# Optimization experiments

Measured on AMD Instinct MI355X. Metric: run time of the kernel, lower is better.

## Reference

```python
import jax, jax.numpy as jnp
import numpy as np
from jax import lax

# dims
B, N, D, H, K, NS = 16, 4096, 64, 128, 32, 1024  # clouds, pts/cloud, feat, hidden, max neighbors, fps samples
R = 0.2  # radius


def _fps(pos, n_s):
    """Farthest point sampling on one cloud. pos: [N,3] -> idx [n_s] int32."""
    n = pos.shape[0]

    def step(carry, _):
        dist, last = carry
        d = jnp.sum((pos - pos[last]) ** 2, axis=-1)
        dist = jnp.minimum(dist, d)
        nxt = jnp.argmax(dist).astype(jnp.int32)
        return (dist, nxt), last

    init = (jnp.full((n,), 1e10, pos.dtype), jnp.int32(0))
    _, idx = lax.scan(step, init, None, length=n_s)
    return idx


def setup_inputs() -> dict:
    key = jax.random.key(0)
    ks = jax.random.split(key, 6)
    s1 = 1.0 / np.sqrt(D + 1)
    s2 = 1.0 / np.sqrt(H)
    s3 = 1.0 / np.sqrt(D + H)
    return {
        "x": jax.random.normal(ks[0], (B, N, D), jnp.float32),
        "pos": jax.random.uniform(ks[1], (B, N, 3), jnp.float32),
        "W1": jax.random.normal(ks[2], (D + 1, H), jnp.float32) * s1,
        "b1": jnp.zeros((H,), jnp.float32),
        "W2": jax.random.normal(ks[3], (H, 3), jnp.float32) * s2,
        "b2": jnp.zeros((3,), jnp.float32),
        "W3": jax.random.normal(ks[4], (D + H, H), jnp.float32) * s3,
        "b3": jnp.zeros((H,), jnp.float32),
    }


def reference(x, pos, W1, b1, W2, b2, W3, b3):
    # 1) FPS downsample per cloud -> centers
    idx = jax.vmap(lambda p: _fps(p, NS))(pos)                    # [B,NS]
    pos_s = jax.vmap(lambda p, i: p[i])(pos, idx)                 # [B,NS,3]

    # 2) radius neighbor search: nearest-K within R (<= max_num_neighbors=32)
    d2 = jnp.sum((pos_s[:, :, None, :] - pos[:, None, :, :]) ** 2, axis=-1)  # [B,NS,N]
    masked = jnp.where(d2 <= R * R, d2, jnp.inf)
    neg, nbr = lax.top_k(-masked, K)                              # nearest K
    valid = (-neg) <= R * R                                       # [B,NS,K]

    # 3) gather neighbor features/positions
    x_j = jax.vmap(lambda a, i: a[i])(x, nbr)                     # [B,NS,K,D]
    pos_j = jax.vmap(lambda a, i: a[i])(pos, nbr)                 # [B,NS,K,3]
    diff = pos_j - pos_s[:, :, None, :]                           # pos_j - pos_i
    d2sel = jnp.sum(diff ** 2, axis=-1)
    dist = jnp.where(d2sel > 0, jnp.sqrt(jnp.where(d2sel > 0, d2sel, 1.0)), 0.0)

    # 4) message MLPs
    feat = jnp.concatenate([x_j, dist[..., None]], axis=-1)       # [B,NS,K,D+1]
    emb = jax.nn.relu(feat @ W1 + b1)                             # nn_msg_x
    pw = emb @ W2 + b2                                            # nn_msg_pos
    pmsg = diff * pw

    # 5) masked aggregate: sum for x, mean for pos
    m = valid[..., None].astype(emb.dtype)
    aggr_x = jnp.sum(emb * m, axis=2)                             # [B,NS,H]
    cnt = jnp.maximum(jnp.sum(m, axis=2), 1.0)                    # [B,NS,1]
    aggr_pos = jnp.sum(pmsg * m, axis=2) / cnt                    # [B,NS,3]

    # 6) update
    x_d = jax.vmap(lambda a, i: a[i])(x, idx)                     # [B,NS,D]
    out_x = jax.nn.relu(jnp.concatenate([x_d, aggr_x], axis=-1) @ W3 + b3)
    out_pos = pos_s + aggr_pos
    return out_x, out_pos, idx
```

## Files before the change

### kernel.cpp

```cpp
#include <hip/hip_runtime.h>
#include <math.h>

#define B_ 16
#define N_ 4096
#define D_ 64
#define H_ 128
#define K_ 32
#define NS_ 1024
#define R2_ 0.04f
#define NCAP_ 256
#define NBR_GRID_ ((B_ * NS_) / 4)

typedef short short8 __attribute__((ext_vector_type(8)));
typedef float f32x4 __attribute__((ext_vector_type(4)));
typedef unsigned short ushort_t;

static __device__ __forceinline__ short f2bf(float f) {
    unsigned u = __float_as_uint(f);
    unsigned r = (u + 0x7FFFu + ((u >> 16) & 1u)) >> 16;
    return (short)r;
}

template<int CTRL, int RM>
static __device__ __forceinline__ unsigned dppmov(unsigned v) {
    return (unsigned)__builtin_amdgcn_update_dpp((int)v, (int)v, CTRL, RM, 0xF, false);
}

#define DPP_FMAX_STEP(CTRL, RM)                                           \
    {                                                                     \
        float n = __uint_as_float(dppmov<CTRL, RM>(__float_as_uint(wm))); \
        wm = fmaxf(wm, n);                                                \
    }

#define DPP_UMIN_STEP(CTRL, RM)                                           \
    {                                                                     \
        unsigned n = dppmov<CTRL, RM>(cand);                              \
        cand = n < cand ? n : cand;                                       \
    }

#define DPP_UMIN_STEP_V(var, CTRL, RM)                                    \
    {                                                                     \
        unsigned n = dppmov<CTRL, RM>(var);                               \
        var = n < var ? n : var;                                          \
    }

__global__ __launch_bounds__(256, 1) void fps_kernel(
    const float* __restrict__ pos, int* __restrict__ idx_i,
    float* __restrict__ idx_f, float* __restrict__ pos_s)
{
    __shared__ float4 lpos4[N_];
    __shared__ float4 sres[NS_];
    __shared__ unsigned long long skey[2][4];
    __shared__ float4 scoord[2][4];
    const int b = blockIdx.x;
    const int t = threadIdx.x;
    const int wv = t >> 6;
    const int lane = t & 63;
    const float* posb = pos + (size_t)b * N_ * 3;
    for (int p = t; p < N_; p += 256)
        lpos4[p] = make_float4(posb[3 * p + 0], posb[3 * p + 1], posb[3 * p + 2], 0.f);
    __syncthreads();

    float px[16], py[16], pz[16], dist[16];
#pragma unroll
    for (int j = 0; j < 16; ++j) {
        float4 v = lpos4[t + 256 * j];
        px[j] = v.x; py[j] = v.y; pz[j] = v.z;
        dist[j] = 1e10f;
    }
    unsigned curidx = 0;
    float4 c0 = lpos4[0];
    float ccx = c0.x, ccy = c0.y, ccz = c0.z;

    for (int ns = 0; ns < NS_; ++ns) {
        if (t == 0)
            sres[ns] = make_float4(ccx, ccy, ccz, __uint_as_float(curidx));
        float bv = -1.f; int bj = 0;
#pragma unroll
        for (int j = 0; j < 16; ++j) {
            float dx = __fsub_rn(px[j], ccx);
            float dy = __fsub_rn(py[j], ccy);
            float dz = __fsub_rn(pz[j], ccz);
            float d2 = __fadd_rn(__fadd_rn(__fmul_rn(dx, dx), __fmul_rn(dy, dy)), __fmul_rn(dz, dz));
            float dn = fminf(dist[j], d2);
            dist[j] = dn;
            bool g = dn > bv;
            bv = g ? dn : bv;
            bj = g ? j : bj;
        }
        float wm = bv;
        DPP_FMAX_STEP(0x111, 0xF)
        DPP_FMAX_STEP(0x112, 0xF)
        DPP_FMAX_STEP(0x114, 0xF)
        DPP_FMAX_STEP(0x118, 0xF)
        DPP_FMAX_STEP(0x142, 0xA)
        DPP_FMAX_STEP(0x143, 0xC)
        const float wavemax = __uint_as_float(
            (unsigned)__builtin_amdgcn_readlane((int)__float_as_uint(wm), 63));
        const unsigned pidx = (unsigned)t + ((unsigned)bj << 8);
        const unsigned long long mask = __ballot(bv == wavemax);
        unsigned widx;
        if (__popcll(mask) == 1) {
            const int wl = __ffsll((long long)mask) - 1;
            widx = (unsigned)__builtin_amdgcn_readlane((int)pidx, wl);
        } else {
            unsigned cand = (bv == wavemax) ? pidx : 0xFFFFFFFFu;
            DPP_UMIN_STEP(0x111, 0xF)
            DPP_UMIN_STEP(0x112, 0xF)
            DPP_UMIN_STEP(0x114, 0xF)
            DPP_UMIN_STEP(0x118, 0xF)
            DPP_UMIN_STEP(0x142, 0xA)
            DPP_UMIN_STEP(0x143, 0xC)
            widx = (unsigned)__builtin_amdgcn_readlane((int)cand, 63);
        }
        float4 wc = lpos4[widx];
        if (lane == 0) {
            skey[ns & 1][wv] = (((unsigned long long)__float_as_uint(wavemax)) << 32)
                             | (unsigned long long)(0xFFFFFFFFu - widx);
            scoord[ns & 1][wv] = wc;
        }
        __syncthreads();
        {
            unsigned sid = (unsigned)(lane & 3);
            unsigned long long skv = skey[ns & 1][sid];
            float4 scv = scoord[ns & 1][sid];
            unsigned kh2 = (unsigned)(skv >> 32), kl2 = (unsigned)skv;
#define SLOT_STEP(CTRL)                                                        \
            {                                                                  \
                unsigned nh = dppmov<CTRL, 0xF>(kh2);                          \
                unsigned nl = dppmov<CTRL, 0xF>(kl2);                          \
                unsigned nsid = dppmov<CTRL, 0xF>(sid);                        \
                unsigned long long nk = (((unsigned long long)nh) << 32) | nl; \
                unsigned long long ok = (((unsigned long long)kh2) << 32) | kl2;\
                if (nk > ok) { kh2 = nh; kl2 = nl; sid = nsid; }               \
            }
            SLOT_STEP(0x101)
            SLOT_STEP(0x102)
#undef SLOT_STEP
            const int slotwin = __builtin_amdgcn_readfirstlane((int)sid);
            curidx = 0xFFFFFFFFu - (unsigned)__builtin_amdgcn_readfirstlane((int)kl2);
            ccx = __uint_as_float((unsigned)__builtin_amdgcn_readlane(
                      (int)__float_as_uint(scv.x), slotwin));
            ccy = __uint_as_float((unsigned)__builtin_amdgcn_readlane(
                      (int)__float_as_uint(scv.y), slotwin));
            ccz = __uint_as_float((unsigned)__builtin_amdgcn_readlane(
                      (int)__float_as_uint(scv.z), slotwin));
        }
    }
    __syncthreads();
    for (int i = t; i < NS_; i += 256) {
        float4 r = sres[i];
        unsigned id = __float_as_uint(r.w);
        idx_i[b * NS_ + i] = (int)id;
        idx_f[b * NS_ + i] = (float)id;
        pos_s[(b * NS_ + i) * 3 + 0] = r.x;
        pos_s[(b * NS_ + i) * 3 + 1] = r.y;
        pos_s[(b * NS_ + i) * 3 + 2] = r.z;
    }
}

__global__ __launch_bounds__(256) void nbr_kernel(
    const float* __restrict__ pos, const float* __restrict__ pos_s,
    int* __restrict__ nbr, float* __restrict__ cntv,
    const float* __restrict__ x, ushort_t* __restrict__ xb)
{
    __shared__ unsigned long long ck[4][NCAP_];
    if (blockIdx.x >= NBR_GRID_) {
        const size_t i = ((size_t)(blockIdx.x - NBR_GRID_) * 256 + threadIdx.x) * 8;
        float4 a = *(const float4*)(x + i);
        float4 c = *(const float4*)(x + i + 4);
        short8 o;
        o[0] = f2bf(a.x); o[1] = f2bf(a.y); o[2] = f2bf(a.z); o[3] = f2bf(a.w);
        o[4] = f2bf(c.x); o[5] = f2bf(c.y); o[6] = f2bf(c.z); o[7] = f2bf(c.w);
        *(short8*)(xb + i) = o;
        return;
    }
    const int w = threadIdx.x >> 6;
    const int lane = threadIdx.x & 63;
    const int s = blockIdx.x * 4 + w;
    const int b = s >> 10;
    const float cx = pos_s[s * 3 + 0], cy = pos_s[s * 3 + 1], cz = pos_s[s * 3 + 2];
    const float* posb = pos + (size_t)b * N_ * 3;
    int m = 0;
    for (int base = 0; base < N_; base += 64) {
        int p = base + lane;
        float dx = __fsub_rn(posb[3 * p + 0], cx);
        float dy = __fsub_rn(posb[3 * p + 1], cy);
        float dz = __fsub_rn(posb[3 * p + 2], cz);
        float d2 = __fadd_rn(__fadd_rn(__fmul_rn(dx, dx), __fmul_rn(dy, dy)), __fmul_rn(dz, dz));
        bool in = (d2 <= R2_);
        unsigned long long msk = __ballot(in);
        int before = __popcll(msk & ((1ull << lane) - 1ull));
        int slot = m + before;
        if (in && slot < NCAP_)
            ck[w][slot] = ((unsigned long long)__float_as_uint(d2) << 32) | (unsigned)p;
        m += __popcll(msk);
    }
    __asm__ volatile("s_waitcnt lgkmcnt(0)" ::: "memory");
    int kcnt = m < K_ ? m : K_;
    if (m <= NCAP_) {
        unsigned long long kr[4];
#pragma unroll
        for (int r = 0; r < 4; ++r) {
            int q = r * 64 + lane;
            unsigned long long v = ck[w][q & (NCAP_ - 1)];
            kr[r] = (q < m) ? v : ~0ull;
        }
        unsigned chosen = 0;
        for (int k = 0; k < kcnt; ++k) {
            unsigned long long localk = ~0ull; int br = -1;
#pragma unroll
            for (int r = 0; r < 4; ++r) {
                bool ok = (!((chosen >> r) & 1u)) && (kr[r] < localk);
                localk = ok ? kr[r] : localk;
                br = ok ? r : br;
            }
            const unsigned mybits = (unsigned)(localk >> 32);
            const unsigned myidx = (unsigned)localk;
            unsigned wb = mybits;
            DPP_UMIN_STEP_V(wb, 0x111, 0xF)
            DPP_UMIN_STEP_V(wb, 0x112, 0xF)
            DPP_UMIN_STEP_V(wb, 0x114, 0xF)
            DPP_UMIN_STEP_V(wb, 0x118, 0xF)
            DPP_UMIN_STEP_V(wb, 0x142, 0xA)
            DPP_UMIN_STEP_V(wb, 0x143, 0xC)
            const unsigned minbits = (unsigned)__builtin_amdgcn_readlane((int)wb, 63);
            const unsigned long long wmask = __ballot(mybits == minbits);
            unsigned widx;
            if (__popcll(wmask) == 1) {
                const int wl = __ffsll((long long)wmask) - 1;
                widx = (unsigned)__builtin_amdgcn_readlane((int)myidx, wl);
            } else {
                unsigned cand = (mybits == minbits) ? myidx : 0xFFFFFFFFu;
                DPP_UMIN_STEP(0x111, 0xF)
                DPP_UMIN_STEP(0x112, 0xF)
                DPP_UMIN_STEP(0x114, 0xF)
                DPP_UMIN_STEP(0x118, 0xF)
                DPP_UMIN_STEP(0x142, 0xA)
                DPP_UMIN_STEP(0x143, 0xC)
                widx = (unsigned)__builtin_amdgcn_readlane((int)cand, 63);
            }
            if (mybits == minbits && myidx == widx) chosen |= 1u << br;
            if (lane == 0) nbr[s * K_ + k] = (int)widx;
        }
    } else {
        unsigned long long prev = 0ull;
        for (int k = 0; k < kcnt; ++k) {
            unsigned long long localk = ~0ull;
            for (int base = 0; base < N_; base += 64) {
                int p = base + lane;
                float dx = __fsub_rn(posb[3 * p + 0], cx);
                float dy = __fsub_rn(posb[3 * p + 1], cy);
                float dz = __fsub_rn(posb[3 * p + 2], cz);
                float d2 = __fadd_rn(__fadd_rn(__fmul_rn(dx, dx), __fmul_rn(dy, dy)), __fmul_rn(dz, dz));
                if (d2 <= R2_) {
                    unsigned long long key =
                        ((unsigned long long)__float_as_uint(d2) << 32) | (unsigned)p;
                    if (key >= prev && key < localk) localk = key;
                }
            }
            unsigned kh = (unsigned)(localk >> 32), kl = (unsigned)localk;
#define DPP_MIN_STEP2(CTRL, RM)                                           \
            {                                                             \
                unsigned nh = dppmov<CTRL, RM>(kh);                       \
                unsigned nl = dppmov<CTRL, RM>(kl);                       \
                unsigned long long nk = (((unsigned long long)nh) << 32) | nl; \
                unsigned long long ok = (((unsigned long long)kh) << 32) | kl; \
                if (nk < ok) { kh = nh; kl = nl; }                        \
            }
            DPP_MIN_STEP2(0x111, 0xF)
            DPP_MIN_STEP2(0x112, 0xF)
            DPP_MIN_STEP2(0x114, 0xF)
            DPP_MIN_STEP2(0x118, 0xF)
            DPP_MIN_STEP2(0x142, 0xA)
            DPP_MIN_STEP2(0x143, 0xC)
#undef DPP_MIN_STEP2
            unsigned mh = (unsigned)__builtin_amdgcn_readlane((int)kh, 63);
            unsigned ml = (unsigned)__builtin_amdgcn_readlane((int)kl, 63);
            unsigned long long bk = (((unsigned long long)mh) << 32) | ml;
            prev = bk + 1ull;
            if (lane == 0) nbr[s * K_ + k] = (int)(bk & 0xFFFFFFFFull);
        }
    }
    if (lane == 0) {
        for (int k = kcnt; k < K_; ++k) nbr[s * K_ + k] = -1;
        cntv[s] = (float)kcnt;
    }
}

__global__ __launch_bounds__(256) void msg_kernel(
    const ushort_t* __restrict__ xb, const float* __restrict__ pos,
    const float* __restrict__ W1, const float* __restrict__ b1,
    const float* __restrict__ W2, const float* __restrict__ b2,
    const float* __restrict__ pos_s, const int* __restrict__ nbr,
    const float* __restrict__ cntv, float* __restrict__ aggr_x,
    float* __restrict__ out_pos)
{
    __shared__ __align__(16) char smem[4 * 5120];
    const int t = threadIdx.x;
    const int wv = t >> 6, lane = t & 63;
    const int quad = lane >> 4, cl = lane & 15;
    char* wb = smem + wv * 5120;

    short8 bfrag[8][2];
    float b1v[8], w1dv[8], w2v0[8], w2v1[8], w2v2[8];
#pragma unroll
    for (int Nt = 0; Nt < 8; ++Nt) {
        const int h = Nt * 16 + cl;
#pragma unroll
        for (int ks = 0; ks < 2; ++ks) {
            short8 f;
#pragma unroll
            for (int jj = 0; jj < 8; ++jj)
                f[jj] = f2bf(W1[(ks * 32 + quad * 8 + jj) * H_ + h]);
            bfrag[Nt][ks] = f;
        }
        b1v[Nt] = b1[h];
        w1dv[Nt] = W1[64 * H_ + h];
        w2v0[Nt] = W2[h * 3 + 0];
        w2v1[Nt] = W2[h * 3 + 1];
        w2v2[Nt] = W2[h * 3 + 2];
    }
    const float b20 = b2[0], b21 = b2[1], b22 = b2[2];

    const int kkg = lane >> 1, half = lane & 1;
    for (int i = 0; i < 4; ++i) {
        const int s = blockIdx.x * 16 + wv * 4 + i;
        const int b = s >> 10;
        const int n = nbr[s * K_ + kkg];
        {
            char* frow = wb + kkg * 144 + half * 64;
            if (n >= 0) {
                const short8* xr = (const short8*)(xb + ((size_t)b * N_ + n) * D_) + half * 4;
#pragma unroll
                for (int q = 0; q < 4; ++q) *(short8*)(frow + q * 16) = xr[q];
            } else {
                short8 z = {0, 0, 0, 0, 0, 0, 0, 0};
#pragma unroll
                for (int q = 0; q < 4; ++q) *(short8*)(frow + q * 16) = z;
            }
            if (half == 0) {
                float dxm = 0.f, dym = 0.f, dzm = 0.f, de = -1.f;
                if (n >= 0) {
                    const float* pj = pos + ((size_t)b * N_ + n) * 3;
                    float dx = pj[0] - pos_s[s * 3 + 0];
                    float dy = pj[1] - pos_s[s * 3 + 1];
                    float dz = pj[2] - pos_s[s * 3 + 2];
                    float d2 = dx * dx + dy * dy + dz * dz;
                    de = d2 > 0.f ? sqrtf(d2) : 0.f;
                    dxm = dx; dym = dy; dzm = dz;
                }
                f32x4 sv = {dxm, dym, dzm, de};
                *(f32x4*)(wb + 4608 + kkg * 16) = sv;
            }
        }
        float agp[8] = {0, 0, 0, 0, 0, 0, 0, 0};
        float gp0[8] = {0, 0, 0, 0, 0, 0, 0, 0};
        float gp1[8] = {0, 0, 0, 0, 0, 0, 0, 0};
        float gp2[8] = {0, 0, 0, 0, 0, 0, 0, 0};
#pragma unroll
        for (int Mt = 0; Mt < 2; ++Mt) {
            short8 a0 = *(short8*)(wb + (Mt * 16 + cl) * 144 + quad * 16);
            short8 a1 = *(short8*)(wb + (Mt * 16 + cl) * 144 + 64 + quad * 16);
            f32x4 acc[8];
#pragma unroll
            for (int Nt = 0; Nt < 8; ++Nt) {
                f32x4 z = {0.f, 0.f, 0.f, 0.f};
                z = __builtin_amdgcn_mfma_f32_16x16x32_bf16(a0, bfrag[Nt][0], z, 0, 0, 0);
                z = __builtin_amdgcn_mfma_f32_16x16x32_bf16(a1, bfrag[Nt][1], z, 0, 0, 0);
                acc[Nt] = z;
            }
            f32x4 sd[4];
#pragma unroll
            for (int r = 0; r < 4; ++r)
                sd[r] = *(f32x4*)(wb + 4608 + (Mt * 16 + quad * 4 + r) * 16);
#pragma unroll
            for (int Nt = 0; Nt < 8; ++Nt) {
#pragma unroll
                for (int r = 0; r < 4; ++r) {
                    float dr = sd[r][3];
                    float wgt = dr >= 0.f ? 1.f : 0.f;
                    float dd = dr >= 0.f ? dr : 0.f;
                    float e = fmaf(dd, w1dv[Nt], acc[Nt][r]) + b1v[Nt];
                    e = e > 0.f ? e : 0.f;
                    agp[Nt] = fmaf(wgt, e, agp[Nt]);
                    gp0[Nt] = fmaf(sd[r][0], e, gp0[Nt]);
                    gp1[Nt] = fmaf(sd[r][1], e, gp1[Nt]);
                    gp2[Nt] = fmaf(sd[r][2], e, gp2[Nt]);
                }
            }
        }
#pragma unroll
        for (int Nt = 0; Nt < 8; ++Nt) {
            float v = agp[Nt]; v += __shfl_xor(v, 16); v += __shfl_xor(v, 32);
            aggr_x[(size_t)s * H_ + Nt * 16 + cl] = v;
            float g0 = gp0[Nt]; g0 += __shfl_xor(g0, 16); g0 += __shfl_xor(g0, 32); gp0[Nt] = g0;
            float g1 = gp1[Nt]; g1 += __shfl_xor(g1, 16); g1 += __shfl_xor(g1, 32); gp1[Nt] = g1;
            float g2 = gp2[Nt]; g2 += __shfl_xor(g2, 16); g2 += __shfl_xor(g2, 32); gp2[Nt] = g2;
        }
        float pr0 = 0.f, pr1 = 0.f, pr2 = 0.f;
#pragma unroll
        for (int Nt = 0; Nt < 8; ++Nt) {
            pr0 = fmaf(w2v0[Nt], gp0[Nt], pr0);
            pr1 = fmaf(w2v1[Nt], gp1[Nt], pr1);
            pr2 = fmaf(w2v2[Nt], gp2[Nt], pr2);
        }
#pragma unroll
        for (int off = 1; off < 16; off <<= 1) {
            pr0 += __shfl_xor(pr0, off);
            pr1 += __shfl_xor(pr1, off);
            pr2 += __shfl_xor(pr2, off);
        }
        f32x4 dsv = *(f32x4*)(wb + 4608 + (lane & 31) * 16);
        float q0 = dsv[0], q1 = dsv[1], q2 = dsv[2];
#pragma unroll
        for (int off = 1; off < 32; off <<= 1) {
            q0 += __shfl_xor(q0, off);
            q1 += __shfl_xor(q1, off);
            q2 += __shfl_xor(q2, off);
        }
        float cnt = cntv[s]; if (cnt < 1.f) cnt = 1.f;
        if (lane < 3) {
            float pr = lane == 0 ? pr0 : (lane == 1 ? pr1 : pr2);
            float qq = lane == 0 ? q0 : (lane == 1 ? q1 : q2);
            float bb = lane == 0 ? b20 : (lane == 1 ? b21 : b22);
            out_pos[s * 3 + lane] = pos_s[s * 3 + lane] + (pr + bb * qq) / cnt;
        }
    }
}

__global__ __launch_bounds__(128) void out_kernel(
    const float* __restrict__ x, const float* __restrict__ W3,
    const float* __restrict__ b3, const int* __restrict__ idx_i,
    const float* __restrict__ aggr_x, float* __restrict__ out_x)
{
    __shared__ float rows[32][208];
    const int t = threadIdx.x;
    const int s0 = blockIdx.x * 32;
    const int sl = t >> 2, part = t & 3;
    const int s = s0 + sl;
    const int b = s >> 10;
    const int id = idx_i[s];
    {
        const float4* xr = (const float4*)(x + ((size_t)b * N_ + id) * D_);
        float4* rr = (float4*)&rows[sl][0];
#pragma unroll
        for (int q = 0; q < 4; ++q) rr[part * 4 + q] = xr[part * 4 + q];
        const float4* ar = (const float4*)(aggr_x + (size_t)s * H_);
        float4* rr2 = (float4*)&rows[sl][64];
#pragma unroll
        for (int q = 0; q < 8; ++q) rr2[part * 8 + q] = ar[part * 8 + q];
    }
    __syncthreads();
    float acc[32];
#pragma unroll
    for (int i = 0; i < 32; ++i) acc[i] = 0.f;
    for (int j4 = 0; j4 < 48; ++j4) {
        float w0 = W3[(j4 * 4 + 0) * H_ + t];
        float w1 = W3[(j4 * 4 + 1) * H_ + t];
        float w2 = W3[(j4 * 4 + 2) * H_ + t];
        float w3 = W3[(j4 * 4 + 3) * H_ + t];
#pragma unroll
        for (int i = 0; i < 32; ++i) {
            const float4 f = *(const float4*)&rows[i][j4 * 4];
            float a = acc[i];
            a = fmaf(f.x, w0, a); a = fmaf(f.y, w1, a);
            a = fmaf(f.z, w2, a); a = fmaf(f.w, w3, a);
            acc[i] = a;
        }
    }
    const float bb = b3[t];
#pragma unroll
    for (int i = 0; i < 32; ++i) {
        float v = acc[i] + bb;
        v = v > 0.f ? v : 0.f;
        out_x[(size_t)(s0 + i) * H_ + t] = v;
    }
}

extern "C" void kernel_launch(void* const* d_in, const int* in_sizes, int n_in,
                              void* d_out, int out_size, void* d_ws, size_t ws_size,
                              hipStream_t stream) {
    const float* x   = (const float*)d_in[0];
    const float* pos = (const float*)d_in[1];
    const float* W1  = (const float*)d_in[2];
    const float* b1  = (const float*)d_in[3];
    const float* W2  = (const float*)d_in[4];
    const float* b2  = (const float*)d_in[5];
    const float* W3  = (const float*)d_in[6];
    const float* b3  = (const float*)d_in[7];

    float* out_x   = (float*)d_out;
    float* out_pos = (float*)d_out + 2097152;
    float* idx_f   = (float*)d_out + 2146304;

    char* ws = (char*)d_ws;
    int*      idx_i  = (int*)ws;
    float*    pos_s  = (float*)(ws + 65536);
    int*      nbr    = (int*)(ws + 262144);
    float*    cntv   = (float*)(ws + 2359296);
    float*    aggr_x = (float*)(ws + 2424832);
    ushort_t* x_bf16 = (ushort_t*)(ws + 10813440);

    fps_kernel<<<B_, 256, 0, stream>>>(pos, idx_i, idx_f, pos_s);
    nbr_kernel<<<NBR_GRID_ + (B_ * N_ * D_) / (256 * 8), 256, 0, stream>>>(
        pos, pos_s, nbr, cntv, x, x_bf16);
    msg_kernel<<<(B_ * NS_) / 16, 256, 0, stream>>>(x_bf16, pos, W1, b1, W2, b2,
                                                    pos_s, nbr, cntv, aggr_x, out_pos);
    out_kernel<<<(B_ * NS_) / 32, 128, 0, stream>>>(x, W3, b3, idx_i, aggr_x, out_x);
}
```

Before: 920.3 us.

## Fuse FPS with neighbor search via producer-consumer progress counters

Merges the FPS and neighbor-search/bf16-convert kernels into one persistent launch. Sixteen blocks run FPS and publish every 64 sampled centers through an atomic progress counter with release semantics. 224 consumer blocks first convert x to bf16, then spin on the counters and run the radius search for centers as they become ready. This overlaps the long serial FPS with neighbor search and the conversion, at the cost of spin-wait polling, a memset launch, and a risk of deadlock if the producer blocks are not all resident at once.

```diff
diff --git a/kernel.cpp b/kernel.cpp
--- a/kernel.cpp
+++ b/kernel.cpp
@@ -9,7 +9,9 @@
 #define NS_ 1024
 #define R2_ 0.04f
 #define NCAP_ 256
-#define NBR_GRID_ ((B_ * NS_) / 4)
+#define NCONS_ 224
+#define CVT_UNITS_ 2048
+#define NBR_UNITS_ 4096
 
 typedef short short8 __attribute__((ext_vector_type(8)));
 typedef float f32x4 __attribute__((ext_vector_type(4)));
@@ -44,14 +46,153 @@
         var = n < var ? n : var;                                          \
     }
 
-__global__ __launch_bounds__(256, 1) void fps_kernel(
+__global__ __launch_bounds__(256, 1) void mega_kernel(
     const float* __restrict__ pos, int* __restrict__ idx_i,
-    float* __restrict__ idx_f, float* __restrict__ pos_s)
+    float* __restrict__ idx_f, float* __restrict__ pos_s,
+    const float* __restrict__ x, ushort_t* __restrict__ xb,
+    int* __restrict__ nbr, float* __restrict__ cntv,
+    int* __restrict__ prog)
 {
     __shared__ float4 lpos4[N_];
     __shared__ float4 sres[NS_];
     __shared__ unsigned long long skey[2][4];
     __shared__ float4 scoord[2][4];
+    __shared__ unsigned long long ck[4][NCAP_];
+
+    if (blockIdx.x >= B_) {
+        const int cid = (int)blockIdx.x - B_;
+        const int t = threadIdx.x;
+        for (int u = cid; u < CVT_UNITS_; u += NCONS_) {
+            const size_t i = ((size_t)u * 256 + t) * 8;
+            float4 a = *(const float4*)(x + i);
+            float4 c = *(const float4*)(x + i + 4);
+            short8 o;
+            o[0] = f2bf(a.x); o[1] = f2bf(a.y); o[2] = f2bf(a.z); o[3] = f2bf(a.w);
+            o[4] = f2bf(c.x); o[5] = f2bf(c.y); o[6] = f2bf(c.z); o[7] = f2bf(c.w);
+            *(short8*)(xb + i) = o;
+        }
+        const int w = t >> 6;
+        const int lane = t & 63;
+        for (int u = cid; u < NBR_UNITS_; u += NCONS_) {
+            const int s = u * 4 + w;
+            const int bcl = s >> 10;
+            const int need = (s & (NS_ - 1)) + 1;
+            while (__hip_atomic_load(&prog[bcl], __ATOMIC_ACQUIRE,
+                                     __HIP_MEMORY_SCOPE_AGENT) < need)
+                __builtin_amdgcn_s_sleep(64);
+            const float cx = pos_s[s * 3 + 0];
+            const float cy = pos_s[s * 3 + 1];
+            const float cz = pos_s[s * 3 + 2];
+            const float* posb2 = pos + (size_t)bcl * N_ * 3;
+            int m = 0;
+            for (int base = 0; base < N_; base += 64) {
+                int p = base + lane;
+                float dx = __fsub_rn(posb2[3 * p + 0], cx);
+                float dy = __fsub_rn(posb2[3 * p + 1], cy);
+                float dz = __fsub_rn(posb2[3 * p + 2], cz);
+                float d2 = __fadd_rn(__fadd_rn(__fmul_rn(dx, dx), __fmul_rn(dy, dy)), __fmul_rn(dz, dz));
+                bool in = (d2 <= R2_);
+                unsigned long long msk = __ballot(in);
+                int before = __popcll(msk & ((1ull << lane) - 1ull));
+                int slot = m + before;
+                if (in && slot < NCAP_)
+                    ck[w][slot] = ((unsigned long long)__float_as_uint(d2) << 32) | (unsigned)p;
+                m += __popcll(msk);
+            }
+            __asm__ volatile("s_waitcnt lgkmcnt(0)" ::: "memory");
+            int kcnt = m < K_ ? m : K_;
+            if (m <= NCAP_) {
+                unsigned long long kr[4];
+#pragma unroll
+                for (int r = 0; r < 4; ++r) {
+                    int q = r * 64 + lane;
+                    unsigned long long v = ck[w][q & (NCAP_ - 1)];
+                    kr[r] = (q < m) ? v : ~0ull;
+                }
+                unsigned chosen = 0;
+                for (int k = 0; k < kcnt; ++k) {
+                    unsigned long long localk = ~0ull; int br = -1;
+#pragma unroll
+                    for (int r = 0; r < 4; ++r) {
+                        bool ok = (!((chosen >> r) & 1u)) && (kr[r] < localk);
+                        localk = ok ? kr[r] : localk;
+                        br = ok ? r : br;
+                    }
+                    const unsigned mybits = (unsigned)(localk >> 32);
+                    const unsigned myidx = (unsigned)localk;
+                    unsigned wb = mybits;
+                    DPP_UMIN_STEP_V(wb, 0x111, 0xF)
+                    DPP_UMIN_STEP_V(wb, 0x112, 0xF)
+                    DPP_UMIN_STEP_V(wb, 0x114, 0xF)
+                    DPP_UMIN_STEP_V(wb, 0x118, 0xF)
+                    DPP_UMIN_STEP_V(wb, 0x142, 0xA)
+                    DPP_UMIN_STEP_V(wb, 0x143, 0xC)
+                    const unsigned minbits = (unsigned)__builtin_amdgcn_readlane((int)wb, 63);
+                    const unsigned long long wmask = __ballot(mybits == minbits);
+                    unsigned widx;
+                    if (__popcll(wmask) == 1) {
+                        const int wl = __ffsll((long long)wmask) - 1;
+                        widx = (unsigned)__builtin_amdgcn_readlane((int)myidx, wl);
+                    } else {
+                        unsigned cand = (mybits == minbits) ? myidx : 0xFFFFFFFFu;
+                        DPP_UMIN_STEP(0x111, 0xF)
+                        DPP_UMIN_STEP(0x112, 0xF)
+                        DPP_UMIN_STEP(0x114, 0xF)
+                        DPP_UMIN_STEP(0x118, 0xF)
+                        DPP_UMIN_STEP(0x142, 0xA)
+                        DPP_UMIN_STEP(0x143, 0xC)
+                        widx = (unsigned)__builtin_amdgcn_readlane((int)cand, 63);
+                    }
+                    if (mybits == minbits && myidx == widx) chosen |= 1u << br;
+                    if (lane == 0) nbr[s * K_ + k] = (int)widx;
+                }
+            } else {
+                unsigned long long prev = 0ull;
+                for (int k = 0; k < kcnt; ++k) {
+                    unsigned long long localk = ~0ull;
+                    for (int base = 0; base < N_; base += 64) {
+                        int p = base + lane;
+                        float dx = __fsub_rn(posb2[3 * p + 0], cx);
+                        float dy = __fsub_rn(posb2[3 * p + 1], cy);
+                        float dz = __fsub_rn(posb2[3 * p + 2], cz);
+                        float d2 = __fadd_rn(__fadd_rn(__fmul_rn(dx, dx), __fmul_rn(dy, dy)), __fmul_rn(dz, dz));
+                        if (d2 <= R2_) {
+                            unsigned long long key =
+                                ((unsigned long long)__float_as_uint(d2) << 32) | (unsigned)p;
+                            if (key >= prev && key < localk) localk = key;
+                        }
+                    }
+                    unsigned kh = (unsigned)(localk >> 32), kl = (unsigned)localk;
+#define DPP_MIN_STEP2(CTRL, RM)                                           \
+                    {                                                     \
+                        unsigned nh = dppmov<CTRL, RM>(kh);               \
+                        unsigned nl = dppmov<CTRL, RM>(kl);               \
+                        unsigned long long nk = (((unsigned long long)nh) << 32) | nl; \
+                        unsigned long long ok = (((unsigned long long)kh) << 32) | kl; \
+                        if (nk < ok) { kh = nh; kl = nl; }                \
+                    }
+                    DPP_MIN_STEP2(0x111, 0xF)
+                    DPP_MIN_STEP2(0x112, 0xF)
+                    DPP_MIN_STEP2(0x114, 0xF)
+                    DPP_MIN_STEP2(0x118, 0xF)
+                    DPP_MIN_STEP2(0x142, 0xA)
+                    DPP_MIN_STEP2(0x143, 0xC)
+#undef DPP_MIN_STEP2
+                    unsigned mh = (unsigned)__builtin_amdgcn_readlane((int)kh, 63);
+                    unsigned ml = (unsigned)__builtin_amdgcn_readlane((int)kl, 63);
+                    unsigned long long bk = (((unsigned long long)mh) << 32) | ml;
+                    prev = bk + 1ull;
+                    if (lane == 0) nbr[s * K_ + k] = (int)(bk & 0xFFFFFFFFull);
+                }
+            }
+            if (lane == 0) {
+                for (int k = kcnt; k < K_; ++k) nbr[s * K_ + k] = -1;
+                cntv[s] = (float)kcnt;
+            }
+        }
+        return;
+    }
+
     const int b = blockIdx.x;
     const int t = threadIdx.x;
     const int wv = t >> 6;
@@ -146,145 +287,23 @@
             ccz = __uint_as_float((unsigned)__builtin_amdgcn_readlane(
                       (int)__float_as_uint(scv.z), slotwin));
         }
-    }
-    __syncthreads();
-    for (int i = t; i < NS_; i += 256) {
-        float4 r = sres[i];
-        unsigned id = __float_as_uint(r.w);
-        idx_i[b * NS_ + i] = (int)id;
-        idx_f[b * NS_ + i] = (float)id;
-        pos_s[(b * NS_ + i) * 3 + 0] = r.x;
-        pos_s[(b * NS_ + i) * 3 + 1] = r.y;
-        pos_s[(b * NS_ + i) * 3 + 2] = r.z;
-    }
-}
-
-__global__ __launch_bounds__(256) void nbr_kernel(
-    const float* __restrict__ pos, const float* __restrict__ pos_s,
-    int* __restrict__ nbr, float* __restrict__ cntv,
-    const float* __restrict__ x, ushort_t* __restrict__ xb)
-{
-    __shared__ unsigned long long ck[4][NCAP_];
-    if (blockIdx.x >= NBR_GRID_) {
-        const size_t i = ((size_t)(blockIdx.x - NBR_GRID_) * 256 + threadIdx.x) * 8;
-        float4 a = *(const float4*)(x + i);
-        float4 c = *(const float4*)(x + i + 4);
-        short8 o;
-        o[0] = f2bf(a.x); o[1] = f2bf(a.y); o[2] = f2bf(a.z); o[3] = f2bf(a.w);
-        o[4] = f2bf(c.x); o[5] = f2bf(c.y); o[6] = f2bf(c.z); o[7] = f2bf(c.w);
-        *(short8*)(xb + i) = o;
-        return;
-    }
-    const int w = threadIdx.x >> 6;
-    const int lane = threadIdx.x & 63;
-    const int s = blockIdx.x * 4 + w;
-    const int b = s >> 10;
-    const float cx = pos_s[s * 3 + 0], cy = pos_s[s * 3 + 1], cz = pos_s[s * 3 + 2];
-    const float* posb = pos + (size_t)b * N_ * 3;
-    int m = 0;
-    for (int base = 0; base < N_; base += 64) {
-        int p = base + lane;
-        float dx = __fsub_rn(posb[3 * p + 0], cx);
-        float dy = __fsub_rn(posb[3 * p + 1], cy);
-        float dz = __fsub_rn(posb[3 * p + 2], cz);
-        float d2 = __fadd_rn(__fadd_rn(__fmul_rn(dx, dx), __fmul_rn(dy, dy)), __fmul_rn(dz, dz));
-        bool in = (d2 <= R2_);
-        unsigned long long msk = __ballot(in);
-        int before = __popcll(msk & ((1ull << lane) - 1ull));
-        int slot = m + before;
-        if (in && slot < NCAP_)
-            ck[w][slot] = ((unsigned long long)__float_as_uint(d2) << 32) | (unsigned)p;
-        m += __popcll(msk);
-    }
-    __asm__ volatile("s_waitcnt lgkmcnt(0)" ::: "memory");
-    int kcnt = m < K_ ? m : K_;
-    if (m <= NCAP_) {
-        unsigned long long kr[4];
-#pragma unroll
-        for (int r = 0; r < 4; ++r) {
-            int q = r * 64 + lane;
-            unsigned long long v = ck[w][q & (NCAP_ - 1)];
-            kr[r] = (q < m) ? v : ~0ull;
-        }
-        unsigned chosen = 0;
-        for (int k = 0; k < kcnt; ++k) {
-            unsigned long long localk = ~0ull; int br = -1;
-#pragma unroll
-            for (int r = 0; r < 4; ++r) {
-                bool ok = (!((chosen >> r) & 1u)) && (kr[r] < localk);
-                localk = ok ? kr[r] : localk;
-                br = ok ? r : br;
-            }
-            const unsigned mybits = (unsigned)(localk >> 32);
-            const unsigned myidx = (unsigned)localk;
-            unsigned wb = mybits;
-            DPP_UMIN_STEP_V(wb, 0x111, 0xF)
-            DPP_UMIN_STEP_V(wb, 0x112, 0xF)
-            DPP_UMIN_STEP_V(wb, 0x114, 0xF)
-            DPP_UMIN_STEP_V(wb, 0x118, 0xF)
-            DPP_UMIN_STEP_V(wb, 0x142, 0xA)
-            DPP_UMIN_STEP_V(wb, 0x143, 0xC)
-            const unsigned minbits = (unsigned)__builtin_amdgcn_readlane((int)wb, 63);
-            const unsigned long long wmask = __ballot(mybits == minbits);
-            unsigned widx;
-            if (__popcll(wmask) == 1) {
-                const int wl = __ffsll((long long)wmask) - 1;
-                widx = (unsigned)__builtin_amdgcn_readlane((int)myidx, wl);
-            } else {
-                unsigned cand = (mybits == minbits) ? myidx : 0xFFFFFFFFu;
-                DPP_UMIN_STEP(0x111, 0xF)
-                DPP_UMIN_STEP(0x112, 0xF)
-                DPP_UMIN_STEP(0x114, 0xF)
-                DPP_UMIN_STEP(0x118, 0xF)
-                DPP_UMIN_STEP(0x142, 0xA)
-                DPP_UMIN_STEP(0x143, 0xC)
-                widx = (unsigned)__builtin_amdgcn_readlane((int)cand, 63);
-            }
-            if (mybits == minbits && myidx == widx) chosen |= 1u << br;
-            if (lane == 0) nbr[s * K_ + k] = (int)widx;
-        }
-    } else {
-        unsigned long long prev = 0ull;
-        for (int k = 0; k < kcnt; ++k) {
-            unsigned long long localk = ~0ull;
-            for (int base = 0; base < N_; base += 64) {
-                int p = base + lane;
-                float dx = __fsub_rn(posb[3 * p + 0], cx);
-                float dy = __fsub_rn(posb[3 * p + 1], cy);
-                float dz = __fsub_rn(posb[3 * p + 2], cz);
-                float d2 = __fadd_rn(__fadd_rn(__fmul_rn(dx, dx), __fmul_rn(dy, dy)), __fmul_rn(dz, dz));
-                if (d2 <= R2_) {
-                    unsigned long long key =
-                        ((unsigned long long)__float_as_uint(d2) << 32) | (unsigned)p;
-                    if (key >= prev && key < localk) localk = key;
-                }
-            }
-            unsigned kh = (unsigned)(localk >> 32), kl = (unsigned)localk;
-#define DPP_MIN_STEP2(CTRL, RM)                                           \
-            {                                                             \
-                unsigned nh = dppmov<CTRL, RM>(kh);                       \
-                unsigned nl = dppmov<CTRL, RM>(kl);                       \
-                unsigned long long nk = (((unsigned long long)nh) << 32) | nl; \
-                unsigned long long ok = (((unsigned long long)kh) << 32) | kl; \
-                if (nk < ok) { kh = nh; kl = nl; }                        \
-            }
-            DPP_MIN_STEP2(0x111, 0xF)
-            DPP_MIN_STEP2(0x112, 0xF)
-            DPP_MIN_STEP2(0x114, 0xF)
-            DPP_MIN_STEP2(0x118, 0xF)
-            DPP_MIN_STEP2(0x142, 0xA)
-            DPP_MIN_STEP2(0x143, 0xC)
-#undef DPP_MIN_STEP2
-            unsigned mh = (unsigned)__builtin_amdgcn_readlane((int)kh, 63);
-            unsigned ml = (unsigned)__builtin_amdgcn_readlane((int)kl, 63);
-            unsigned long long bk = (((unsigned long long)mh) << 32) | ml;
-            prev = bk + 1ull;
-            if (lane == 0) nbr[s * K_ + k] = (int)(bk & 0xFFFFFFFFull);
-        }
-    }
-    if (lane == 0) {
-        for (int k = kcnt; k < K_; ++k) nbr[s * K_ + k] = -1;
-        cntv[s] = (float)kcnt;
+        if ((ns & 63) == 63) {
+            if (t < 64) {
+                const int i = (ns & ~63) + t;
+                float4 r = sres[i];
+                unsigned id = __float_as_uint(r.w);
+                idx_i[b * NS_ + i] = (int)id;
+                idx_f[b * NS_ + i] = (float)id;
+                pos_s[(b * NS_ + i) * 3 + 0] = r.x;
+                pos_s[(b * NS_ + i) * 3 + 1] = r.y;
+                pos_s[(b * NS_ + i) * 3 + 2] = r.z;
+                __threadfence();
+            }
+            __syncthreads();
+            if (t == 0)
+                __hip_atomic_fetch_add(&prog[b], 64, __ATOMIC_RELEASE,
+                                       __HIP_MEMORY_SCOPE_AGENT);
+        }
     }
 }
 
@@ -501,10 +520,11 @@
     float*    cntv   = (float*)(ws + 2359296);
     float*    aggr_x = (float*)(ws + 2424832);
     ushort_t* x_bf16 = (ushort_t*)(ws + 10813440);
-
-    fps_kernel<<<B_, 256, 0, stream>>>(pos, idx_i, idx_f, pos_s);
-    nbr_kernel<<<NBR_GRID_ + (B_ * N_ * D_) / (256 * 8), 256, 0, stream>>>(
-        pos, pos_s, nbr, cntv, x, x_bf16);
+    int*      prog   = (int*)(ws + 44367872);
+
+    hipMemsetAsync(prog, 0, 64, stream);
+    mega_kernel<<<B_ + NCONS_, 256, 0, stream>>>(pos, idx_i, idx_f, pos_s,
+                                                 x, x_bf16, nbr, cntv, prog);
     msg_kernel<<<(B_ * NS_) / 16, 256, 0, stream>>>(x_bf16, pos, W1, b1, W2, b2,
                                                     pos_s, nbr, cntv, aggr_x, out_pos);
     out_kernel<<<(B_ * NS_) / 32, 128, 0, stream>>>(x, W3, b3, idx_i, aggr_x, out_x);
```

Result: slower. 1.316 ms (+43.0%).

## Split FPS into two phases and overlap neighbor search with the second phase

Applied to the files above, without the earlier changes.

FPS is split at iteration 576. The first kernel saves the per-thread distance state and the current center to workspace. A second kernel resumes FPS in 16 blocks while its extra blocks run the radius neighbor search for the first 576 centers and the bf16 conversion of x, using the otherwise idle CUs. A final kernel handles the neighbors of the remaining centers. This hides part of the serial, latency-bound FPS behind the neighbor work, at the cost of one more launch and a state spill and reload. The FPS blocks may also face contention or scheduling delay from the co-resident blocks.

```diff
diff --git a/kernel.cpp b/kernel.cpp
--- a/kernel.cpp
+++ b/kernel.cpp
@@ -9,7 +9,10 @@
 #define NS_ 1024
 #define R2_ 0.04f
 #define NCAP_ 256
-#define NBR_GRID_ ((B_ * NS_) / 4)
+#define SPLIT_ 576
+#define NBRA_BLOCKS_ 2304
+#define NBRB_BLOCKS_ 1792
+#define CVT_BLOCKS_ 2048
 
 typedef short short8 __attribute__((ext_vector_type(8)));
 typedef float f32x4 __attribute__((ext_vector_type(4)));
@@ -44,9 +47,87 @@
         var = n < var ? n : var;                                          \
     }
 
-__global__ __launch_bounds__(256, 1) void fps_kernel(
+#define FPS_ITER_BODY()                                                          \
+    {                                                                            \
+        if (t == 0)                                                              \
+            sres[ns] = make_float4(ccx, ccy, ccz, __uint_as_float(curidx));      \
+        float bv = -1.f; int bj = 0;                                             \
+        _Pragma("unroll")                                                        \
+        for (int j = 0; j < 16; ++j) {                                           \
+            float dx = __fsub_rn(px[j], ccx);                                    \
+            float dy = __fsub_rn(py[j], ccy);                                    \
+            float dz = __fsub_rn(pz[j], ccz);                                    \
+            float d2 = __fadd_rn(__fadd_rn(__fmul_rn(dx, dx), __fmul_rn(dy, dy)), __fmul_rn(dz, dz)); \
+            float dn = fminf(dist[j], d2);                                       \
+            dist[j] = dn;                                                        \
+            bool g = dn > bv;                                                    \
+            bv = g ? dn : bv;                                                    \
+            bj = g ? j : bj;                                                     \
+        }                                                                        \
+        float wm = bv;                                                           \
+        DPP_FMAX_STEP(0x111, 0xF)                                                \
+        DPP_FMAX_STEP(0x112, 0xF)                                                \
+        DPP_FMAX_STEP(0x114, 0xF)                                                \
+        DPP_FMAX_STEP(0x118, 0xF)                                                \
+        DPP_FMAX_STEP(0x142, 0xA)                                                \
+        DPP_FMAX_STEP(0x143, 0xC)                                                \
+        const float wavemax = __uint_as_float(                                   \
+            (unsigned)__builtin_amdgcn_readlane((int)__float_as_uint(wm), 63));  \
+        const unsigned pidx = (unsigned)t + ((unsigned)bj << 8);                 \
+        const unsigned long long mask = __ballot(bv == wavemax);                 \
+        unsigned widx;                                                           \
+        if (__popcll(mask) == 1) {                                               \
+            const int wl = __ffsll((long long)mask) - 1;                         \
+            widx = (unsigned)__builtin_amdgcn_readlane((int)pidx, wl);           \
+        } else {                                                                 \
+            unsigned cand = (bv == wavemax) ? pidx : 0xFFFFFFFFu;                \
+            DPP_UMIN_STEP(0x111, 0xF)                                            \
+            DPP_UMIN_STEP(0x112, 0xF)                                            \
+            DPP_UMIN_STEP(0x114, 0xF)                                            \
+            DPP_UMIN_STEP(0x118, 0xF)                                            \
+            DPP_UMIN_STEP(0x142, 0xA)                                            \
+            DPP_UMIN_STEP(0x143, 0xC)                                            \
+            widx = (unsigned)__builtin_amdgcn_readlane((int)cand, 63);           \
+        }                                                                        \
+        float4 wc = lpos4[widx];                                                 \
+        if (lane == 0) {                                                         \
+            skey[ns & 1][wv] = (((unsigned long long)__float_as_uint(wavemax)) << 32) \
+                             | (unsigned long long)(0xFFFFFFFFu - widx);         \
+            scoord[ns & 1][wv] = wc;                                             \
+        }                                                                        \
+        __syncthreads();                                                         \
+        {                                                                        \
+            unsigned sid = (unsigned)(lane & 3);                                 \
+            unsigned long long skv = skey[ns & 1][sid];                          \
+            float4 scv = scoord[ns & 1][sid];                                    \
+            unsigned kh2 = (unsigned)(skv >> 32), kl2 = (unsigned)skv;           \
+            SLOT_STEP(0x101)                                                     \
+            SLOT_STEP(0x102)                                                     \
+            const int slotwin = __builtin_amdgcn_readfirstlane((int)sid);        \
+            curidx = 0xFFFFFFFFu - (unsigned)__builtin_amdgcn_readfirstlane((int)kl2); \
+            ccx = __uint_as_float((unsigned)__builtin_amdgcn_readlane(           \
+                      (int)__float_as_uint(scv.x), slotwin));                    \
+            ccy = __uint_as_float((unsigned)__builtin_amdgcn_readlane(           \
+                      (int)__float_as_uint(scv.y), slotwin));                    \
+            ccz = __uint_as_float((unsigned)__builtin_amdgcn_readlane(           \
+                      (int)__float_as_uint(scv.z), slotwin));                    \
+        }                                                                        \
+    }
+
+#define SLOT_STEP(CTRL)                                                        \
+            {                                                                  \
+                unsigned nh = dppmov<CTRL, 0xF>(kh2);                          \
+                unsigned nl = dppmov<CTRL, 0xF>(kl2);                          \
+                unsigned nsid = dppmov<CTRL, 0xF>(sid);                        \
+                unsigned long long nk = (((unsigned long long)nh) << 32) | nl; \
+                unsigned long long ok = (((unsigned long long)kh2) << 32) | kl2;\
+                if (nk > ok) { kh2 = nh; kl2 = nl; sid = nsid; }               \
+            }
+
+__global__ __launch_bounds__(256, 1) void fps1_kernel(
     const float* __restrict__ pos, int* __restrict__ idx_i,
-    float* __restrict__ idx_f, float* __restrict__ pos_s)
+    float* __restrict__ idx_f, float* __restrict__ pos_s,
+    float* __restrict__ dstate, float4* __restrict__ cstate)
 {
     __shared__ float4 lpos4[N_];
     __shared__ float4 sres[NS_];
@@ -72,83 +153,11 @@
     float4 c0 = lpos4[0];
     float ccx = c0.x, ccy = c0.y, ccz = c0.z;
 
-    for (int ns = 0; ns < NS_; ++ns) {
-        if (t == 0)
-            sres[ns] = make_float4(ccx, ccy, ccz, __uint_as_float(curidx));
-        float bv = -1.f; int bj = 0;
-#pragma unroll
-        for (int j = 0; j < 16; ++j) {
-            float dx = __fsub_rn(px[j], ccx);
-            float dy = __fsub_rn(py[j], ccy);
-            float dz = __fsub_rn(pz[j], ccz);
-            float d2 = __fadd_rn(__fadd_rn(__fmul_rn(dx, dx), __fmul_rn(dy, dy)), __fmul_rn(dz, dz));
-            float dn = fminf(dist[j], d2);
-            dist[j] = dn;
-            bool g = dn > bv;
-            bv = g ? dn : bv;
-            bj = g ? j : bj;
-        }
-        float wm = bv;
-        DPP_FMAX_STEP(0x111, 0xF)
-        DPP_FMAX_STEP(0x112, 0xF)
-        DPP_FMAX_STEP(0x114, 0xF)
-        DPP_FMAX_STEP(0x118, 0xF)
-        DPP_FMAX_STEP(0x142, 0xA)
-        DPP_FMAX_STEP(0x143, 0xC)
-        const float wavemax = __uint_as_float(
-            (unsigned)__builtin_amdgcn_readlane((int)__float_as_uint(wm), 63));
-        const unsigned pidx = (unsigned)t + ((unsigned)bj << 8);
-        const unsigned long long mask = __ballot(bv == wavemax);
-        unsigned widx;
-        if (__popcll(mask) == 1) {
-            const int wl = __ffsll((long long)mask) - 1;
-            widx = (unsigned)__builtin_amdgcn_readlane((int)pidx, wl);
-        } else {
-            unsigned cand = (bv == wavemax) ? pidx : 0xFFFFFFFFu;
-            DPP_UMIN_STEP(0x111, 0xF)
-            DPP_UMIN_STEP(0x112, 0xF)
-            DPP_UMIN_STEP(0x114, 0xF)
-            DPP_UMIN_STEP(0x118, 0xF)
-            DPP_UMIN_STEP(0x142, 0xA)
-            DPP_UMIN_STEP(0x143, 0xC)
-            widx = (unsigned)__builtin_amdgcn_readlane((int)cand, 63);
-        }
-        float4 wc = lpos4[widx];
-        if (lane == 0) {
-            skey[ns & 1][wv] = (((unsigned long long)__float_as_uint(wavemax)) << 32)
-                             | (unsigned long long)(0xFFFFFFFFu - widx);
-            scoord[ns & 1][wv] = wc;
-        }
-        __syncthreads();
-        {
-            unsigned sid = (unsigned)(lane & 3);
-            unsigned long long skv = skey[ns & 1][sid];
-            float4 scv = scoord[ns & 1][sid];
-            unsigned kh2 = (unsigned)(skv >> 32), kl2 = (unsigned)skv;
-#define SLOT_STEP(CTRL)                                                        \
-            {                                                                  \
-                unsigned nh = dppmov<CTRL, 0xF>(kh2);                          \
-                unsigned nl = dppmov<CTRL, 0xF>(kl2);                          \
-                unsigned nsid = dppmov<CTRL, 0xF>(sid);                        \
-                unsigned long long nk = (((unsigned long long)nh) << 32) | nl; \
-                unsigned long long ok = (((unsigned long long)kh2) << 32) | kl2;\
-                if (nk > ok) { kh2 = nh; kl2 = nl; sid = nsid; }               \
-            }
-            SLOT_STEP(0x101)
-            SLOT_STEP(0x102)
-#undef SLOT_STEP
-            const int slotwin = __builtin_amdgcn_readfirstlane((int)sid);
-            curidx = 0xFFFFFFFFu - (unsigned)__builtin_amdgcn_readfirstlane((int)kl2);
-            ccx = __uint_as_float((unsigned)__builtin_amdgcn_readlane(
-                      (int)__float_as_uint(scv.x), slotwin));
-            ccy = __uint_as_float((unsigned)__builtin_amdgcn_readlane(
-                      (int)__float_as_uint(scv.y), slotwin));
-            ccz = __uint_as_float((unsigned)__builtin_amdgcn_readlane(
-                      (int)__float_as_uint(scv.z), slotwin));
-        }
-    }
+    for (int ns = 0; ns < SPLIT_; ++ns)
+        FPS_ITER_BODY()
+
     __syncthreads();
-    for (int i = t; i < NS_; i += 256) {
+    for (int i = t; i < SPLIT_; i += 256) {
         float4 r = sres[i];
         unsigned id = __float_as_uint(r.w);
         idx_i[b * NS_ + i] = (int)id;
@@ -157,30 +166,201 @@
         pos_s[(b * NS_ + i) * 3 + 1] = r.y;
         pos_s[(b * NS_ + i) * 3 + 2] = r.z;
     }
-}
-
-__global__ __launch_bounds__(256) void nbr_kernel(
+#pragma unroll
+    for (int j = 0; j < 16; ++j)
+        dstate[(size_t)(b * 16 + j) * 256 + t] = dist[j];
+    if (t == 0)
+        cstate[b] = make_float4(ccx, ccy, ccz, __uint_as_float(curidx));
+}
+
+__global__ __launch_bounds__(256, 1) void fps2_kernel(
+    const float* __restrict__ pos, int* __restrict__ idx_i,
+    float* __restrict__ idx_f, float* __restrict__ pos_s,
+    const float* __restrict__ dstate, const float4* __restrict__ cstate,
+    const float* __restrict__ x, ushort_t* __restrict__ xb,
+    int* __restrict__ nbr, float* __restrict__ cntv)
+{
+    __shared__ float4 lpos4[N_];
+    __shared__ float4 sres[NS_];
+    __shared__ unsigned long long skey[2][4];
+    __shared__ float4 scoord[2][4];
+    __shared__ unsigned long long ck[4][NCAP_];
+
+    const int t = threadIdx.x;
+    if (blockIdx.x >= B_) {
+        const int cid = (int)blockIdx.x - B_;
+        const int w = t >> 6;
+        const int lane = t & 63;
+        if (cid < NBRA_BLOCKS_) {
+            const int cl = cid / 144;
+            const int ns = (cid % 144) * 4 + w;
+            const int s = cl * NS_ + ns;
+            const float cx = pos_s[s * 3 + 0], cy = pos_s[s * 3 + 1], cz = pos_s[s * 3 + 2];
+            const float* posb2 = pos + (size_t)cl * N_ * 3;
+            int m = 0;
+            for (int base = 0; base < N_; base += 64) {
+                int p = base + lane;
+                float dx = __fsub_rn(posb2[3 * p + 0], cx);
+                float dy = __fsub_rn(posb2[3 * p + 1], cy);
+                float dz = __fsub_rn(posb2[3 * p + 2], cz);
+                float d2 = __fadd_rn(__fadd_rn(__fmul_rn(dx, dx), __fmul_rn(dy, dy)), __fmul_rn(dz, dz));
+                bool in = (d2 <= R2_);
+                unsigned long long msk = __ballot(in);
+                int before = __popcll(msk & ((1ull << lane) - 1ull));
+                int slot = m + before;
+                if (in && slot < NCAP_)
+                    ck[w][slot] = ((unsigned long long)__float_as_uint(d2) << 32) | (unsigned)p;
+                m += __popcll(msk);
+            }
+            __asm__ volatile("s_waitcnt lgkmcnt(0)" ::: "memory");
+            int kcnt = m < K_ ? m : K_;
+            if (m <= NCAP_) {
+                unsigned long long kr[4];
+#pragma unroll
+                for (int r = 0; r < 4; ++r) {
+                    int q = r * 64 + lane;
+                    unsigned long long vk = ck[w][q & (NCAP_ - 1)];
+                    kr[r] = (q < m) ? vk : ~0ull;
+                }
+                unsigned chosen = 0;
+                for (int k = 0; k < kcnt; ++k) {
+                    unsigned long long localk = ~0ull; int br = -1;
+#pragma unroll
+                    for (int r = 0; r < 4; ++r) {
+                        bool ok = (!((chosen >> r) & 1u)) && (kr[r] < localk);
+                        localk = ok ? kr[r] : localk;
+                        br = ok ? r : br;
+                    }
+                    const unsigned mybits = (unsigned)(localk >> 32);
+                    const unsigned myidx = (unsigned)localk;
+                    unsigned wb = mybits;
+                    DPP_UMIN_STEP_V(wb, 0x111, 0xF)
+                    DPP_UMIN_STEP_V(wb, 0x112, 0xF)
+                    DPP_UMIN_STEP_V(wb, 0x114, 0xF)
+                    DPP_UMIN_STEP_V(wb, 0x118, 0xF)
+                    DPP_UMIN_STEP_V(wb, 0x142, 0xA)
+                    DPP_UMIN_STEP_V(wb, 0x143, 0xC)
+                    const unsigned minbits = (unsigned)__builtin_amdgcn_readlane((int)wb, 63);
+                    const unsigned long long wmask = __ballot(mybits == minbits);
+                    unsigned widx;
+                    if (__popcll(wmask) == 1) {
+                        const int wl = __ffsll((long long)wmask) - 1;
+                        widx = (unsigned)__builtin_amdgcn_readlane((int)myidx, wl);
+                    } else {
+                        unsigned cand = (mybits == minbits) ? myidx : 0xFFFFFFFFu;
+                        DPP_UMIN_STEP(0x111, 0xF)
+                        DPP_UMIN_STEP(0x112, 0xF)
+                        DPP_UMIN_STEP(0x114, 0xF)
+                        DPP_UMIN_STEP(0x118, 0xF)
+                        DPP_UMIN_STEP(0x142, 0xA)
+                        DPP_UMIN_STEP(0x143, 0xC)
+                        widx = (unsigned)__builtin_amdgcn_readlane((int)cand, 63);
+                    }
+                    if (mybits == minbits && myidx == widx) chosen |= 1u << br;
+                    if (lane == 0) nbr[s * K_ + k] = (int)widx;
+                }
+            } else {
+                unsigned long long prev = 0ull;
+                for (int k = 0; k < kcnt; ++k) {
+                    unsigned long long localk = ~0ull;
+                    for (int base = 0; base < N_; base += 64) {
+                        int p = base + lane;
+                        float dx = __fsub_rn(posb2[3 * p + 0], cx);
+                        float dy = __fsub_rn(posb2[3 * p + 1], cy);
+                        float dz = __fsub_rn(posb2[3 * p + 2], cz);
+                        float d2 = __fadd_rn(__fadd_rn(__fmul_rn(dx, dx), __fmul_rn(dy, dy)), __fmul_rn(dz, dz));
+                        if (d2 <= R2_) {
+                            unsigned long long key =
+                                ((unsigned long long)__float_as_uint(d2) << 32) | (unsigned)p;
+                            if (key >= prev && key < localk) localk = key;
+                        }
+                    }
+                    unsigned kh = (unsigned)(localk >> 32), kl = (unsigned)localk;
+#define DPP_MIN_STEP2(CTRL, RM)                                           \
+                    {                                                     \
+                        unsigned nh = dppmov<CTRL, RM>(kh);               \
+                        unsigned nl = dppmov<CTRL, RM>(kl);               \
+                        unsigned long long nk = (((unsigned long long)nh) << 32) | nl; \
+                        unsigned long long ok = (((unsigned long long)kh) << 32) | kl; \
+                        if (nk < ok) { kh = nh; kl = nl; }                \
+                    }
+                    DPP_MIN_STEP2(0x111, 0xF)
+                    DPP_MIN_STEP2(0x112, 0xF)
+                    DPP_MIN_STEP2(0x114, 0xF)
+                    DPP_MIN_STEP2(0x118, 0xF)
+                    DPP_MIN_STEP2(0x142, 0xA)
+                    DPP_MIN_STEP2(0x143, 0xC)
+#undef DPP_MIN_STEP2
+                    unsigned mh = (unsigned)__builtin_amdgcn_readlane((int)kh, 63);
+                    unsigned ml = (unsigned)__builtin_amdgcn_readlane((int)kl, 63);
+                    unsigned long long bk = (((unsigned long long)mh) << 32) | ml;
+                    prev = bk + 1ull;
+                    if (lane == 0) nbr[s * K_ + k] = (int)(bk & 0xFFFFFFFFull);
+                }
+            }
+            if (lane == 0) {
+                for (int k = kcnt; k < K_; ++k) nbr[s * K_ + k] = -1;
+                cntv[s] = (float)kcnt;
+            }
+        } else {
+            const int u = cid - NBRA_BLOCKS_;
+            const size_t i = ((size_t)u * 256 + t) * 8;
+            float4 a = *(const float4*)(x + i);
+            float4 c = *(const float4*)(x + i + 4);
+            short8 o;
+            o[0] = f2bf(a.x); o[1] = f2bf(a.y); o[2] = f2bf(a.z); o[3] = f2bf(a.w);
+            o[4] = f2bf(c.x); o[5] = f2bf(c.y); o[6] = f2bf(c.z); o[7] = f2bf(c.w);
+            *(short8*)(xb + i) = o;
+        }
+        return;
+    }
+
+    const int b = blockIdx.x;
+    const int wv = t >> 6;
+    const int lane = t & 63;
+    const float* posb = pos + (size_t)b * N_ * 3;
+    for (int p = t; p < N_; p += 256)
+        lpos4[p] = make_float4(posb[3 * p + 0], posb[3 * p + 1], posb[3 * p + 2], 0.f);
+    __syncthreads();
+
+    float px[16], py[16], pz[16], dist[16];
+#pragma unroll
+    for (int j = 0; j < 16; ++j) {
+        float4 v = lpos4[t + 256 * j];
+        px[j] = v.x; py[j] = v.y; pz[j] = v.z;
+        dist[j] = dstate[(size_t)(b * 16 + j) * 256 + t];
+    }
+    const float4 cs = cstate[b];
+    float ccx = cs.x, ccy = cs.y, ccz = cs.z;
+    unsigned curidx = __float_as_uint(cs.w);
+
+    for (int ns = SPLIT_; ns < NS_; ++ns)
+        FPS_ITER_BODY()
+
+    __syncthreads();
+    for (int i = SPLIT_ + t; i < NS_; i += 256) {
+        float4 r = sres[i];
+        unsigned id = __float_as_uint(r.w);
+        idx_i[b * NS_ + i] = (int)id;
+        idx_f[b * NS_ + i] = (float)id;
+        pos_s[(b * NS_ + i) * 3 + 0] = r.x;
+        pos_s[(b * NS_ + i) * 3 + 1] = r.y;
+        pos_s[(b * NS_ + i) * 3 + 2] = r.z;
+    }
+}
+
+__global__ __launch_bounds__(256) void nbrB_kernel(
     const float* __restrict__ pos, const float* __restrict__ pos_s,
-    int* __restrict__ nbr, float* __restrict__ cntv,
-    const float* __restrict__ x, ushort_t* __restrict__ xb)
+    int* __restrict__ nbr, float* __restrict__ cntv)
 {
     __shared__ unsigned long long ck[4][NCAP_];
-    if (blockIdx.x >= NBR_GRID_) {
-        const size_t i = ((size_t)(blockIdx.x - NBR_GRID_) * 256 + threadIdx.x) * 8;
-        float4 a = *(const float4*)(x + i);
-        float4 c = *(const float4*)(x + i + 4);
-        short8 o;
-        o[0] = f2bf(a.x); o[1] = f2bf(a.y); o[2] = f2bf(a.z); o[3] = f2bf(a.w);
-        o[4] = f2bf(c.x); o[5] = f2bf(c.y); o[6] = f2bf(c.z); o[7] = f2bf(c.w);
-        *(short8*)(xb + i) = o;
-        return;
-    }
     const int w = threadIdx.x >> 6;
     const int lane = threadIdx.x & 63;
-    const int s = blockIdx.x * 4 + w;
-    const int b = s >> 10;
+    const int cl = blockIdx.x / 112;
+    const int ns = SPLIT_ + (blockIdx.x % 112) * 4 + w;
+    const int s = cl * NS_ + ns;
     const float cx = pos_s[s * 3 + 0], cy = pos_s[s * 3 + 1], cz = pos_s[s * 3 + 2];
-    const float* posb = pos + (size_t)b * N_ * 3;
+    const float* posb = pos + (size_t)cl * N_ * 3;
     int m = 0;
     for (int base = 0; base < N_; base += 64) {
         int p = base + lane;
@@ -501,10 +681,13 @@
     float*    cntv   = (float*)(ws + 2359296);
     float*    aggr_x = (float*)(ws + 2424832);
     ushort_t* x_bf16 = (ushort_t*)(ws + 10813440);
-
-    fps_kernel<<<B_, 256, 0, stream>>>(pos, idx_i, idx_f, pos_s);
-    nbr_kernel<<<NBR_GRID_ + (B_ * N_ * D_) / (256 * 8), 256, 0, stream>>>(
-        pos, pos_s, nbr, cntv, x, x_bf16);
+    float*    dstate = (float*)(ws + 44367872);
+    float4*   cstate = (float4*)(ws + 44630016);
+
+    fps1_kernel<<<B_, 256, 0, stream>>>(pos, idx_i, idx_f, pos_s, dstate, cstate);
+    fps2_kernel<<<B_ + NBRA_BLOCKS_ + CVT_BLOCKS_, 256, 0, stream>>>(
+        pos, idx_i, idx_f, pos_s, dstate, cstate, x, x_bf16, nbr, cntv);
+    nbrB_kernel<<<NBRB_BLOCKS_, 256, 0, stream>>>(pos, pos_s, nbr, cntv);
     msg_kernel<<<(B_ * NS_) / 16, 256, 0, stream>>>(x_bf16, pos, W1, b1, W2, b2,
                                                     pos_s, nbr, cntv, aggr_x, out_pos);
     out_kernel<<<(B_ * NS_) / 32, 128, 0, stream>>>(x, W3, b3, idx_i, aggr_x, out_x);
```

Result: no change. 929.3 us (+1.0%).
